# Kernel tuning notes

Hardware: AMD Instinct MI355X
Metric: run time of the kernel (lower is better)

Reference implementation:

```python
import jax, jax.numpy as jnp
import numpy as np

H, W = 16, 16  # input_resolution
NUM_HEADS = 16
DIM = 512


def build_relative_position_index(h, w):
    coords = np.stack(np.meshgrid(np.arange(h), np.arange(w), indexing='ij'))  # [2,h,w]
    cf = coords.reshape(2, -1)
    rel = cf[:, :, None] - cf[:, None, :]            # [2,N,N]
    rel = rel.transpose(1, 2, 0).astype(np.int32)    # [N,N,2]
    rel[:, :, 0] += h - 1
    rel[:, :, 1] += w - 1
    rel[:, :, 0] *= 2 * w - 1
    return jnp.asarray(rel.sum(-1).reshape(-1), dtype=jnp.int32)  # [N*N]


def setup_inputs() -> dict:
    key = jax.random.key(0)
    ks = jax.random.split(key, 6)
    B, N, C = 128, H * W, DIM
    x = jax.random.normal(ks[0], (B, N, C), dtype=jnp.float32)
    qkv_w = jax.random.normal(ks[1], (3 * C, C), dtype=jnp.float32) * (C ** -0.5)
    qkv_b = jax.random.normal(ks[2], (3 * C,), dtype=jnp.float32) * 0.02
    proj_w = jax.random.normal(ks[3], (C, C), dtype=jnp.float32) * (C ** -0.5)
    proj_b = jax.random.normal(ks[4], (C,), dtype=jnp.float32) * 0.02
    bias_table = jax.random.normal(ks[5], ((2 * H - 1) * (2 * W - 1), NUM_HEADS), dtype=jnp.float32) * 0.02
    rel_index = build_relative_position_index(H, W)
    return {"x": x, "qkv_w": qkv_w, "qkv_b": qkv_b, "proj_w": proj_w,
            "proj_b": proj_b, "bias_table": bias_table, "rel_index": rel_index}


def reference(x, qkv_w, qkv_b, proj_w, proj_b, bias_table, rel_index):
    B, N, C = x.shape
    h = NUM_HEADS
    hd = C // h
    scale = hd ** -0.5
    # qkv projection: [B,N,3C] -> [3,B,h,N,hd]
    qkv = (jnp.einsum('bnc,oc->bno', x, qkv_w) + qkv_b)
    qkv = qkv.reshape(B, N, 3, h, hd).transpose(2, 0, 3, 1, 4)
    q, k, v = qkv[0], qkv[1], qkv[2]
    # relative position bias: gather [N*N,h] -> [1,h,N,N]
    bias = bias_table[rel_index].reshape(N, N, h).transpose(2, 0, 1)[None]
    attn = jnp.einsum('bhnd,bhmd->bhnm', q * scale, k) + bias
    attn = jax.nn.softmax(attn, axis=-1)
    out = jnp.einsum('bhnm,bhmd->bhnd', attn, v)     # [B,h,N,hd]
    out = out.transpose(0, 2, 1, 3).reshape(B, N, C)
    return jnp.einsum('bnc,oc->bno', out, proj_w) + proj_b
```

## Files before the change

kernel.cpp:

```cpp
#include <hip/hip_runtime.h>

typedef __bf16 bf16_t;
typedef __bf16 bf16x8 __attribute__((ext_vector_type(8)));
typedef float f32x4 __attribute__((ext_vector_type(4)));

#define MFMA_16x16x32(a, b, c) __builtin_amdgcn_mfma_f32_16x16x32_bf16((a), (b), (c), 0, 0, 0)
#define LOG2E 1.4426950408889634f

__device__ inline bf16x8 cvt8(const float* __restrict__ p) {
  bf16x8 r;
#pragma unroll
  for (int j = 0; j < 8; j++) r[j] = (bf16_t)p[j];
  return r;
}

__device__ inline void load_lds16(const bf16_t* g, bf16_t* l) {
  __builtin_amdgcn_global_load_lds(
      (const __attribute__((address_space(1))) void*)g,
      (__attribute__((address_space(3))) void*)l, 16, 0, 0);
}

__global__ __launch_bounds__(256) void prep_k(
    const float* __restrict__ x, const float* __restrict__ qkv_w,
    const float* __restrict__ proj_w, const float* __restrict__ table,
    const int* __restrict__ rel,
    bf16_t* __restrict__ xbf, bf16_t* __restrict__ wqkvbf,
    bf16_t* __restrict__ wprojbf, float* __restrict__ biasws) {
  const int bid = blockIdx.x;
  if (bid < 8704) {
    size_t base = ((size_t)bid * 256 + threadIdx.x) * 8;
    if (base < 16777216) {
      *(bf16x8*)(xbf + base) = cvt8(x + base);
    } else if (base < 17563648) {
      size_t o = base - 16777216;
      *(bf16x8*)(wqkvbf + o) = cvt8(qkv_w + o);
    } else {
      size_t o = base - 17563648;
      *(bf16x8*)(wprojbf + o) = cvt8(proj_w + o);
    }
  } else {
    int idx = (bid - 8704) * 256 + threadIdx.x;
    int h = idx >> 16;
    int rem = idx & 65535;
    int qb = rem >> 12;
    int ct = (rem >> 8) & 15;
    int L = (rem >> 2) & 63;
    int r = idx & 3;
    int q = qb * 16 + (L & 15);
    int k = ct * 16 + (L >> 4) * 4 + r;
    biasws[idx] = table[rel[q * 256 + k] * 16 + h] * LOG2E;
  }
}

#define PH_OPEN() __builtin_amdgcn_s_setprio(1)

#define PH_CLOSE()                                        \
  do {                                                    \
    __builtin_amdgcn_s_setprio(0);                        \
    asm volatile("s_waitcnt lgkmcnt(0)" ::: "memory");    \
    __builtin_amdgcn_sched_barrier(0);                    \
    __builtin_amdgcn_s_barrier();                         \
    __builtin_amdgcn_sched_barrier(0);                    \
  } while (0)

#define GATE4()                                           \
  do {                                                    \
    __builtin_amdgcn_s_setprio(0);                        \
    asm volatile("s_waitcnt vmcnt(4)" ::: "memory");      \
    __builtin_amdgcn_s_barrier();                         \
    __builtin_amdgcn_sched_barrier(0);                    \
  } while (0)

#define GATE0()                                           \
  do {                                                    \
    __builtin_amdgcn_s_setprio(0);                        \
    asm volatile("s_waitcnt vmcnt(0)" ::: "memory");      \
    __builtin_amdgcn_s_barrier();                         \
    __builtin_amdgcn_sched_barrier(0);                    \
  } while (0)

#define STG2(src, dst, c)                                                        \
  do {                                                                           \
    load_lds16((src) + (c)*16384, (dst) + (c)*2048);                             \
    load_lds16((src) + ((c) + 1) * 16384, (dst) + ((c) + 1) * 2048);             \
  } while (0)

#define RDA2(dst, buf, ibase)                                                    \
  _Pragma("unroll") for (int i = 0; i < 2; ++i) {                                \
    dst[i][0] = *(const bf16x8*)&As[(buf)*8192 + a0 + ((ibase) + i) * 1024];     \
    dst[i][1] = *(const bf16x8*)&As[(buf)*8192 + a1 + ((ibase) + i) * 1024];     \
  }
#define RDB2(dst, buf, jbase)                                                    \
  _Pragma("unroll") for (int j = 0; j < 2; ++j) {                                \
    dst[j][0] = *(const bf16x8*)&Bs[(buf)*8192 + b0 + ((jbase) + j) * 1024];     \
    dst[j][1] = *(const bf16x8*)&Bs[(buf)*8192 + b1 + ((jbase) + j) * 1024];     \
  }

#define MFQ2(Af, Bf, I0, J0)                                                     \
  _Pragma("unroll") for (int i = 0; i < 2; ++i) _Pragma("unroll")                \
      for (int j = 0; j < 2; ++j) {                                              \
    acc[(I0) + i][(J0) + j] =                                                    \
        MFMA_16x16x32(Af[i][0], Bf[j][0], acc[(I0) + i][(J0) + j]);              \
    acc[(I0) + i][(J0) + j] =                                                    \
        MFMA_16x16x32(Af[i][1], Bf[j][1], acc[(I0) + i][(J0) + j]);              \
  }

#define GEMM_SETUP(Ap, Wp)                                                       \
  __shared__ bf16_t As[2 * 8192];                                                \
  __shared__ bf16_t Bs[2 * 8192];                                                \
  const int t = threadIdx.x;                                                     \
  const int w = t >> 6, L = t & 63;                                              \
  const int wm = w >> 1, wn = w & 1;                                             \
  const int lrow = L & 15, lq = L >> 4;                                          \
  const int srow = t >> 3;                                                       \
  const int sslot = (t & 7) ^ (srow & 7);                                        \
  const bf16_t* ga = (Ap) + (size_t)(m0 + srow) * 512 + sslot * 8;               \
  const bf16_t* gb = (Wp) + (size_t)(n0 + srow) * 512 + sslot * 8;               \
  bf16_t* la = As + t * 8;                                                       \
  bf16_t* lb = Bs + t * 8;                                                       \
  const int m8 = (lrow & 7) * 8;                                                 \
  const int a0 = (wm * 64 + lrow) * 64 + ((lq * 8) ^ m8);                        \
  const int a1 = (wm * 64 + lrow) * 64 + ((32 + lq * 8) ^ m8);                   \
  const int b0 = (wn * 64 + lrow) * 64 + ((lq * 8) ^ m8);                        \
  const int b1 = (wn * 64 + lrow) * 64 + ((32 + lq * 8) ^ m8);

#define PROLOGUE()                                                               \
  STG2(ga, la, 0); STG2(ga, la, 2);                                              \
  STG2(gb, lb, 0); STG2(gb, lb, 2);                                              \
  STG2(ga + 64, la + 8192, 0); STG2(ga + 64, la + 8192, 2);                      \
  asm volatile("s_waitcnt vmcnt(4)" ::: "memory");                               \
  __builtin_amdgcn_s_barrier();                                                  \
  __builtin_amdgcn_sched_barrier(0);

#define HALF_STEADY(CUR, LBDST, LADST, GBP, GAP)                                 \
  {                                                                              \
    bf16x8 fal[2][2], fbl[2][2], fah[2][2], fbh[2][2];                           \
    RDA2(fal, CUR, 0); RDB2(fbl, CUR, 0); RDB2(fbh, CUR, 2);                     \
    STG2(GBP, LBDST, 0);                                                         \
    PH_OPEN(); MFQ2(fal, fbl, 0, 0); PH_CLOSE();                                 \
    RDA2(fah, CUR, 2);                                                           \
    STG2(GBP, LBDST, 2);                                                         \
    PH_OPEN(); MFQ2(fal, fbh, 0, 2); PH_CLOSE();                                 \
    STG2(GAP, LADST, 0);                                                         \
    PH_OPEN(); MFQ2(fah, fbh, 2, 2); PH_CLOSE();                                 \
    STG2(GAP, LADST, 2);                                                         \
    PH_OPEN(); MFQ2(fah, fbl, 2, 0); GATE4();                                    \
  }

#define GEMM_LOOP()                                                              \
  {                                                                              \
    const bf16_t* gA = ga + 128;                                       \
    const bf16_t* gB = gb + 64;                                        \
    _Pragma("unroll 1") for (int G = 0; G < 3; ++G) {                            \
      HALF_STEADY(0, lb + 8192, la, gB, gA)                                      \
      HALF_STEADY(1, lb, la + 8192, gB + 64, gA + 64)                            \
      gA += 128; gB += 128;                                                      \
    }                                                                            \
    {            \
      bf16x8 fal[2][2], fbl[2][2], fah[2][2], fbh[2][2];                         \
      RDA2(fal, 0, 0); RDB2(fbl, 0, 0); RDB2(fbh, 0, 2);                         \
      STG2(gB, lb + 8192, 0);                                                    \
      PH_OPEN(); MFQ2(fal, fbl, 0, 0); PH_CLOSE();                               \
      RDA2(fah, 0, 2);                                                           \
      STG2(gB, lb + 8192, 2);                                                    \
      PH_OPEN(); MFQ2(fal, fbh, 0, 2); PH_CLOSE();                               \
      PH_OPEN(); MFQ2(fah, fbh, 2, 2); PH_CLOSE();                               \
      PH_OPEN(); MFQ2(fah, fbl, 2, 0); GATE0();                                  \
    }                                                                            \
    {                               \
      bf16x8 fal[2][2], fbl[2][2], fah[2][2], fbh[2][2];                         \
      RDA2(fal, 1, 0); RDB2(fbl, 1, 0); RDB2(fbh, 1, 2);                         \
      PH_OPEN(); MFQ2(fal, fbl, 0, 0); PH_CLOSE();                               \
      RDA2(fah, 1, 2);                                                           \
      PH_OPEN(); MFQ2(fal, fbh, 0, 2); PH_CLOSE();                               \
      PH_OPEN(); MFQ2(fah, fbh, 2, 2); PH_CLOSE();                               \
      PH_OPEN(); MFQ2(fah, fbl, 2, 0);                                           \
      __builtin_amdgcn_s_setprio(0);                                             \
      __builtin_amdgcn_sched_barrier(0);                                         \
    }                                                                            \
  }

__global__ __launch_bounds__(256, 2) void qkv_gemm128_k(
    const bf16_t* __restrict__ A, const bf16_t* __restrict__ W,
    const float* __restrict__ Bvec,
    bf16_t* __restrict__ qws, bf16_t* __restrict__ kws, bf16_t* __restrict__ vws) {
  const int id = blockIdx.x;
  const int wg = (id & 7) * 384 + (id >> 3);
  const int mt = wg / 12, nt = wg % 12;
  const int m0 = mt * 128, n0 = nt * 128;

  GEMM_SETUP(A, W);

  f32x4 acc[4][4];
#pragma unroll
  for (int jj = 0; jj < 4; ++jj) {
    float bv = Bvec[n0 + wn * 64 + jj * 16 + lrow];
#pragma unroll
    for (int i = 0; i < 4; ++i) acc[i][jj] = (f32x4){bv, bv, bv, bv};
  }

  PROLOGUE();
  GEMM_LOOP();

  const int col0 = n0 + wn * 64;
  const int s = col0 >> 9;
  bf16_t* dst = (s == 0) ? qws : (s == 1) ? kws : vws;
  const float mul = (s == 0) ? 0.17677669529663687f * LOG2E : 1.0f;
#pragma unroll
  for (int jj = 0; jj < 4; ++jj) {
    int o = col0 + jj * 16 + lrow;
    int rem = o & 511;
    int hh = rem >> 5, d = rem & 31;
#pragma unroll
    for (int i = 0; i < 4; ++i) {
#pragma unroll
      for (int r = 0; r < 4; ++r) {
        int m = m0 + wm * 64 + i * 16 + lq * 4 + r;
        int b = m >> 8, n = m & 255;
        dst[(size_t)(((b * 16 + hh) * 256 + n) << 5) + d] =
            (bf16_t)(acc[i][jj][r] * mul);
      }
    }
  }
}

__global__ __launch_bounds__(256, 2) void proj_gemm128_k(
    const bf16_t* __restrict__ A, const bf16_t* __restrict__ W,
    const float* __restrict__ Bvec, float* __restrict__ out) {
  const int id = blockIdx.x;
  const int wg = (id & 7) * 128 + (id >> 3);
  const int mt = wg >> 2, nt = wg & 3;
  const int m0 = mt * 128, n0 = nt * 128;

  GEMM_SETUP(A, W);

  f32x4 acc[4][4];
#pragma unroll
  for (int jj = 0; jj < 4; ++jj) {
    float bv = Bvec[n0 + wn * 64 + jj * 16 + lrow];
#pragma unroll
    for (int i = 0; i < 4; ++i) acc[i][jj] = (f32x4){bv, bv, bv, bv};
  }

  PROLOGUE();
  GEMM_LOOP();

#pragma unroll
  for (int jj = 0; jj < 4; ++jj) {
    int o = n0 + wn * 64 + jj * 16 + lrow;
#pragma unroll
    for (int i = 0; i < 4; ++i) {
#pragma unroll
      for (int r = 0; r < 4; ++r) {
        int m = m0 + wm * 64 + i * 16 + lq * 4 + r;
        out[(size_t)m * 512 + o] = acc[i][jj][r];
      }
    }
  }
}

__global__ __launch_bounds__(256) void attn_k(
    const bf16_t* __restrict__ qws, const bf16_t* __restrict__ kws,
    const bf16_t* __restrict__ vws, const float* __restrict__ biasws,
    bf16_t* __restrict__ aows) {
  __shared__ __align__(16) bf16_t Vs[32 * 264];

  const int bh = blockIdx.x;
  const int h = bh & 15, b = bh >> 4;

  const int t = threadIdx.x;
  const int w = t >> 6, L = t & 63;
  const int lrow = L & 15, lq = L >> 4;

  const bf16_t* kbase = kws + (size_t)bh * 8192;
  const bf16_t* vbase = vws + (size_t)bh * 8192;

#pragma unroll
  for (int c = 0; c < 4; c++) {
    bf16x8 vv = *(const bf16x8*)(vbase + t * 32 + c * 8);
#pragma unroll
    for (int j = 0; j < 8; j++) Vs[(c * 8 + j) * 264 + t] = vv[j];
  }
  __syncthreads();

  const int idxA = ((2 * (lq & 1)) * 16 + lrow) * 4;
  const int idxB = idxA + 64;
  const bool gsel = (lq < 2);

  const float* bbw = biasws + h * 65536 + (w * 4) * 4096;

#pragma unroll 1
  for (int s = 0; s < 4; ++s) {
    const int qrow0 = w * 64 + s * 16;
    const bf16_t* qbase = qws + (size_t)bh * 8192 + qrow0 * 32;
    bf16x8 qf = *(const bf16x8*)(qbase + lrow * 32 + lq * 8);
    const float* bb = bbw + s * 4096;

    f32x4 S[16];
#pragma unroll
    for (int ct = 0; ct < 16; ct++) {
      bf16x8 kf = *(const bf16x8*)(kbase + (ct * 16 + lrow) * 32 + lq * 8);
      f32x4 bi = *(const f32x4*)(bb + ct * 256 + L * 4);
      S[ct] = MFMA_16x16x32(kf, qf, bi);
    }

    f32x4 sv = {};
#pragma unroll
    for (int ct = 0; ct < 16; ct++) {
#pragma unroll
      for (int r = 0; r < 4; r++) {
        float e;
        asm("v_exp_f32 %0, %1" : "=v"(e) : "v"(S[ct][r]));
        S[ct][r] = e;
      }
      sv += S[ct];
    }
    float sm = (sv[0] + sv[1]) + (sv[2] + sv[3]);
    sm += __shfl_xor(sm, 16, 64);
    sm += __shfl_xor(sm, 32, 64);
    const float inv = 1.0f / sm;

    int pd[16][2];
#pragma unroll
    for (int ct = 0; ct < 16; ct++) {
#pragma unroll
      for (int j = 0; j < 2; j++) {
        int d;
        asm("v_cvt_pk_bf16_f32 %0, %1, %2"
            : "=v"(d) : "v"(S[ct][2 * j]), "v"(S[ct][2 * j + 1]));
        pd[ct][j] = d;
      }
    }

    f32x4 O0 = {}, O1 = {};
#pragma unroll
    for (int kt = 0; kt < 8; kt++) {
      int rA0 = __builtin_amdgcn_ds_bpermute(idxA, pd[2 * kt][0]);
      int rA1 = __builtin_amdgcn_ds_bpermute(idxA, pd[2 * kt][1]);
      int rA2 = __builtin_amdgcn_ds_bpermute(idxB, pd[2 * kt][0]);
      int rA3 = __builtin_amdgcn_ds_bpermute(idxB, pd[2 * kt][1]);
      int rB0 = __builtin_amdgcn_ds_bpermute(idxA, pd[2 * kt + 1][0]);
      int rB1 = __builtin_amdgcn_ds_bpermute(idxA, pd[2 * kt + 1][1]);
      int rB2 = __builtin_amdgcn_ds_bpermute(idxB, pd[2 * kt + 1][0]);
      int rB3 = __builtin_amdgcn_ds_bpermute(idxB, pd[2 * kt + 1][1]);
      int4 Di;
      Di.x = gsel ? rA0 : rB0;
      Di.y = gsel ? rA1 : rB1;
      Di.z = gsel ? rA2 : rB2;
      Di.w = gsel ? rA3 : rB3;
      bf16x8 pf = *reinterpret_cast<bf16x8*>(&Di);
      bf16x8 v0 = *(const bf16x8*)&Vs[lrow * 264 + kt * 32 + lq * 8];
      bf16x8 v1 = *(const bf16x8*)&Vs[(16 + lrow) * 264 + kt * 32 + lq * 8];
      O0 = MFMA_16x16x32(pf, v0, O0);
      O1 = MFMA_16x16x32(pf, v1, O1);
    }

    bf16_t* obase = aows + (size_t)(b * 256 + qrow0) * 512 + h * 32;
#pragma unroll
    for (int r = 0; r < 4; r++) {
      float invO = __int_as_float(
          __builtin_amdgcn_ds_bpermute((lq * 4 + r) * 4, __float_as_int(inv)));
      int rl = lq * 4 + r;
      obase[rl * 512 + lrow] = (bf16_t)(O0[r] * invO);
      obase[rl * 512 + 16 + lrow] = (bf16_t)(O1[r] * invO);
    }
  }
}

extern "C" void kernel_launch(void* const* d_in, const int* in_sizes, int n_in,
                              void* d_out, int out_size, void* d_ws, size_t ws_size,
                              hipStream_t stream) {
  (void)in_sizes; (void)n_in; (void)out_size; (void)ws_size;
  const float* x      = (const float*)d_in[0];
  const float* qkv_w  = (const float*)d_in[1];
  const float* qkv_b  = (const float*)d_in[2];
  const float* proj_w = (const float*)d_in[3];
  const float* proj_b = (const float*)d_in[4];
  const float* table  = (const float*)d_in[5];
  const int*   rel    = (const int*)d_in[6];

  const size_t QKV_ELEMS = 16777216;
  bf16_t* qws     = (bf16_t*)d_ws;
  bf16_t* kws     = qws + QKV_ELEMS;
  bf16_t* vws     = kws + QKV_ELEMS;
  float*  biasws  = (float*)(vws + QKV_ELEMS);
  bf16_t* wqkvbf  = (bf16_t*)(biasws + 1048576);
  bf16_t* wprojbf = wqkvbf + 786432;
  bf16_t* xbf     = wprojbf + 262144;
  bf16_t* aows    = xbf;
  float*  out     = (float*)d_out;

  prep_k<<<12800, 256, 0, stream>>>(x, qkv_w, proj_w, table, rel,
                                    xbf, wqkvbf, wprojbf, biasws);
  qkv_gemm128_k<<<3072, 256, 0, stream>>>(xbf, wqkvbf, qkv_b, qws, kws, vws);
  attn_k<<<2048, 256, 0, stream>>>(qws, kws, vws, biasws, aows);
  proj_gemm128_k<<<1024, 256, 0, stream>>>(aows, wprojbf, proj_b, out);
}
```

Baseline: 323.0 us.

## Split attention into per-strip blocks with XCD-aware mapping and pre-normalized probabilities

Each (batch, head) pair now gets four blocks instead of one. Each block handles a 64-row query strip, with one 16-row tile per wave, so the grid grows from 2048 to 8192 blocks. Block IDs are remapped so that strips of the same head land on the same XCD, which is meant to improve L2 reuse of K and V. The LOG2E prescale is dropped and exp2 is replaced with __expf, and probabilities are normalized before the bf16 pack instead of scaling the output. The cost is that the V tile is loaded into LDS four times per head instead of once.

```diff
diff --git a/kernel.cpp b/kernel.cpp
--- a/kernel.cpp
+++ b/kernel.cpp
@@ -5,7 +5,6 @@
 typedef float f32x4 __attribute__((ext_vector_type(4)));
 
 #define MFMA_16x16x32(a, b, c) __builtin_amdgcn_mfma_f32_16x16x32_bf16((a), (b), (c), 0, 0, 0)
-#define LOG2E 1.4426950408889634f
 
 __device__ inline bf16x8 cvt8(const float* __restrict__ p) {
   bf16x8 r;
@@ -48,7 +47,7 @@
     int r = idx & 3;
     int q = qb * 16 + (L & 15);
     int k = ct * 16 + (L >> 4) * 4 + r;
-    biasws[idx] = table[rel[q * 256 + k] * 16 + h] * LOG2E;
+    biasws[idx] = table[rel[q * 256 + k] * 16 + h];
   }
 }
 
@@ -205,7 +204,7 @@
   const int col0 = n0 + wn * 64;
   const int s = col0 >> 9;
   bf16_t* dst = (s == 0) ? qws : (s == 1) ? kws : vws;
-  const float mul = (s == 0) ? 0.17677669529663687f * LOG2E : 1.0f;
+  const float mul = (s == 0) ? 0.17677669529663687f : 1.0f;
 #pragma unroll
   for (int jj = 0; jj < 4; ++jj) {
     int o = col0 + jj * 16 + lrow;
@@ -265,7 +264,11 @@
     bf16_t* __restrict__ aows) {
   __shared__ __align__(16) bf16_t Vs[32 * 264];
 
-  const int bh = blockIdx.x;
+  const int id = blockIdx.x;
+  const int xcd = id & 7;
+  const int jj = id >> 3;
+  const int bh = (jj >> 2) * 8 + xcd;
+  const int strip = jj & 3;
   const int h = bh & 15, b = bh >> 4;
 
   const int t = threadIdx.x;
@@ -287,83 +290,73 @@
   const int idxB = idxA + 64;
   const bool gsel = (lq < 2);
 
-  const float* bbw = biasws + h * 65536 + (w * 4) * 4096;
-
-#pragma unroll 1
-  for (int s = 0; s < 4; ++s) {
-    const int qrow0 = w * 64 + s * 16;
-    const bf16_t* qbase = qws + (size_t)bh * 8192 + qrow0 * 32;
-    bf16x8 qf = *(const bf16x8*)(qbase + lrow * 32 + lq * 8);
-    const float* bb = bbw + s * 4096;
-
-    f32x4 S[16];
-#pragma unroll
-    for (int ct = 0; ct < 16; ct++) {
-      bf16x8 kf = *(const bf16x8*)(kbase + (ct * 16 + lrow) * 32 + lq * 8);
-      f32x4 bi = *(const f32x4*)(bb + ct * 256 + L * 4);
-      S[ct] = MFMA_16x16x32(kf, qf, bi);
+  const int qrow0 = strip * 64 + w * 16;
+  const bf16_t* qbase = qws + (size_t)bh * 8192 + qrow0 * 32;
+  bf16x8 qf = *(const bf16x8*)(qbase + lrow * 32 + lq * 8);
+  const float* bb = biasws + h * 65536 + (strip * 4 + w) * 4096;
+
+  f32x4 S[16];
+#pragma unroll
+  for (int ct = 0; ct < 16; ct++) {
+    bf16x8 kf = *(const bf16x8*)(kbase + (ct * 16 + lrow) * 32 + lq * 8);
+    f32x4 bi = *(const f32x4*)(bb + ct * 256 + L * 4);
+    S[ct] = MFMA_16x16x32(kf, qf, bi);
+  }
+
+  f32x4 sv = {};
+#pragma unroll
+  for (int ct = 0; ct < 16; ct++) {
+#pragma unroll
+    for (int r = 0; r < 4; r++) S[ct][r] = __expf(S[ct][r]);
+    sv += S[ct];
+  }
+  float sm = (sv[0] + sv[1]) + (sv[2] + sv[3]);
+  sm += __shfl_xor(sm, 16, 64);
+  sm += __shfl_xor(sm, 32, 64);
+  const float inv = 1.0f / sm;
+
+  int pd[16][2];
+#pragma unroll
+  for (int ct = 0; ct < 16; ct++) {
+#pragma unroll
+    for (int j = 0; j < 2; j++) {
+      float lo = S[ct][2 * j] * inv;
+      float hi = S[ct][2 * j + 1] * inv;
+      int d;
+      asm("v_cvt_pk_bf16_f32 %0, %1, %2" : "=v"(d) : "v"(lo), "v"(hi));
+      pd[ct][j] = d;
     }
-
-    f32x4 sv = {};
-#pragma unroll
-    for (int ct = 0; ct < 16; ct++) {
-#pragma unroll
-      for (int r = 0; r < 4; r++) {
-        float e;
-        asm("v_exp_f32 %0, %1" : "=v"(e) : "v"(S[ct][r]));
-        S[ct][r] = e;
-      }
-      sv += S[ct];
-    }
-    float sm = (sv[0] + sv[1]) + (sv[2] + sv[3]);
-    sm += __shfl_xor(sm, 16, 64);
-    sm += __shfl_xor(sm, 32, 64);
-    const float inv = 1.0f / sm;
-
-    int pd[16][2];
-#pragma unroll
-    for (int ct = 0; ct < 16; ct++) {
-#pragma unroll
-      for (int j = 0; j < 2; j++) {
-        int d;
-        asm("v_cvt_pk_bf16_f32 %0, %1, %2"
-            : "=v"(d) : "v"(S[ct][2 * j]), "v"(S[ct][2 * j + 1]));
-        pd[ct][j] = d;
-      }
-    }
-
-    f32x4 O0 = {}, O1 = {};
-#pragma unroll
-    for (int kt = 0; kt < 8; kt++) {
-      int rA0 = __builtin_amdgcn_ds_bpermute(idxA, pd[2 * kt][0]);
-      int rA1 = __builtin_amdgcn_ds_bpermute(idxA, pd[2 * kt][1]);
-      int rA2 = __builtin_amdgcn_ds_bpermute(idxB, pd[2 * kt][0]);
-      int rA3 = __builtin_amdgcn_ds_bpermute(idxB, pd[2 * kt][1]);
-      int rB0 = __builtin_amdgcn_ds_bpermute(idxA, pd[2 * kt + 1][0]);
-      int rB1 = __builtin_amdgcn_ds_bpermute(idxA, pd[2 * kt + 1][1]);
-      int rB2 = __builtin_amdgcn_ds_bpermute(idxB, pd[2 * kt + 1][0]);
-      int rB3 = __builtin_amdgcn_ds_bpermute(idxB, pd[2 * kt + 1][1]);
-      int4 Di;
-      Di.x = gsel ? rA0 : rB0;
-      Di.y = gsel ? rA1 : rB1;
-      Di.z = gsel ? rA2 : rB2;
-      Di.w = gsel ? rA3 : rB3;
-      bf16x8 pf = *reinterpret_cast<bf16x8*>(&Di);
-      bf16x8 v0 = *(const bf16x8*)&Vs[lrow * 264 + kt * 32 + lq * 8];
-      bf16x8 v1 = *(const bf16x8*)&Vs[(16 + lrow) * 264 + kt * 32 + lq * 8];
-      O0 = MFMA_16x16x32(pf, v0, O0);
-      O1 = MFMA_16x16x32(pf, v1, O1);
-    }
-
-    bf16_t* obase = aows + (size_t)(b * 256 + qrow0) * 512 + h * 32;
-#pragma unroll
-    for (int r = 0; r < 4; r++) {
-      float invO = __int_as_float(
-          __builtin_amdgcn_ds_bpermute((lq * 4 + r) * 4, __float_as_int(inv)));
-      int rl = lq * 4 + r;
-      obase[rl * 512 + lrow] = (bf16_t)(O0[r] * invO);
-      obase[rl * 512 + 16 + lrow] = (bf16_t)(O1[r] * invO);
-    }
+  }
+
+  f32x4 O0 = {}, O1 = {};
+#pragma unroll
+  for (int kt = 0; kt < 8; kt++) {
+    int rA0 = __builtin_amdgcn_ds_bpermute(idxA, pd[2 * kt][0]);
+    int rA1 = __builtin_amdgcn_ds_bpermute(idxA, pd[2 * kt][1]);
+    int rA2 = __builtin_amdgcn_ds_bpermute(idxB, pd[2 * kt][0]);
+    int rA3 = __builtin_amdgcn_ds_bpermute(idxB, pd[2 * kt][1]);
+    int rB0 = __builtin_amdgcn_ds_bpermute(idxA, pd[2 * kt + 1][0]);
+    int rB1 = __builtin_amdgcn_ds_bpermute(idxA, pd[2 * kt + 1][1]);
+    int rB2 = __builtin_amdgcn_ds_bpermute(idxB, pd[2 * kt + 1][0]);
+    int rB3 = __builtin_amdgcn_ds_bpermute(idxB, pd[2 * kt + 1][1]);
+    int4 Di;
+    Di.x = gsel ? rA0 : rB0;
+    Di.y = gsel ? rA1 : rB1;
+    Di.z = gsel ? rA2 : rB2;
+    Di.w = gsel ? rA3 : rB3;
+    bf16x8 pf = *reinterpret_cast<bf16x8*>(&Di);
+    bf16x8 v0 = *(const bf16x8*)&Vs[lrow * 264 + kt * 32 + lq * 8];
+    bf16x8 v1 = *(const bf16x8*)&Vs[(16 + lrow) * 264 + kt * 32 + lq * 8];
+    O0 = MFMA_16x16x32(pf, v0, O0);
+    O1 = MFMA_16x16x32(pf, v1, O1);
+  }
+
+  bf16_t* obase = aows + (size_t)(b * 256 + qrow0) * 512 + h * 32;
+#pragma unroll
+  for (int r = 0; r < 4; r++) {
+    int rl = lq * 4 + r;
+    obase[rl * 512 + lrow] = (bf16_t)(O0[r]);
+    obase[rl * 512 + 16 + lrow] = (bf16_t)(O1[r]);
   }
 }
 
@@ -393,6 +386,6 @@
   prep_k<<<12800, 256, 0, stream>>>(x, qkv_w, proj_w, table, rel,
                                     xbf, wqkvbf, wprojbf, biasws);
   qkv_gemm128_k<<<3072, 256, 0, stream>>>(xbf, wqkvbf, qkv_b, qws, kws, vws);
-  attn_k<<<2048, 256, 0, stream>>>(qws, kws, vws, biasws, aows);
+  attn_k<<<8192, 256, 0, stream>>>(qws, kws, vws, biasws, aows);
   proj_gemm128_k<<<1024, 256, 0, stream>>>(aows, wprojbf, proj_b, out);
 }
```

New measurement: 302.7 us. 1.07x faster.
